# Performance work log

Measured on AMD Instinct MI355X. Metric: run time of the kernel, lower is better.

Reference implementation:

```python
import jax, jax.numpy as jnp
import numpy as np

N_NODES = 100000
N_EDGES = 1600000
NFEAT = 128
NHID = 64
DROPOUT = 0.5


def setup_inputs() -> dict:
    key = jax.random.key(0)
    k1, k2, k3, k4, k5, k6 = jax.random.split(key, 6)
    x = jax.random.normal(k1, (N_NODES, NFEAT), dtype=jnp.float32)
    edge_row = jax.random.randint(k2, (N_EDGES,), 0, N_NODES, dtype=jnp.int32)
    edge_col = jax.random.randint(k3, (N_EDGES,), 0, N_NODES, dtype=jnp.int32)
    edge_val = jax.random.uniform(k4, (N_EDGES,), dtype=jnp.float32)
    # GraphConvolution params (uniform init as in Kipf's reference impl)
    stdv = 1.0 / np.sqrt(NHID)
    W = jax.random.uniform(k5, (NFEAT, NHID), minval=-stdv, maxval=stdv, dtype=jnp.float32)
    b = jax.random.uniform(k6, (NHID,), minval=-stdv, maxval=stdv, dtype=jnp.float32)
    return {"x": x, "edge_row": edge_row, "edge_col": edge_col,
            "edge_val": edge_val, "W": W, "b": b}


def reference(x, edge_row, edge_col, edge_val, W, b):
    # GraphConvolution: support = x @ W ; out = spmm(adj, support) + b
    support = x @ W                                   # [N, nhid]
    msgs = edge_val[:, None] * support[edge_col]       # gather: [E, nhid]
    agg = jax.ops.segment_sum(msgs, edge_row, num_segments=N_NODES)  # scatter-add
    h = jax.nn.relu(agg + b)
    # F.dropout(p=0.5, training=True): inverted dropout with fixed mask
    keep = 1.0 - DROPOUT
    mask = jax.random.bernoulli(jax.random.key(42), keep, h.shape)
    return jnp.where(mask, h / keep, 0.0)
```

## Files before the change

### kernel.cpp

```cpp
#include <hip/hip_runtime.h>

#define N_NODES 100000
#define N_EDGES 1600000
#define NFEAT 128
#define NHID 64

#define BBITS 8
#define NBUCK 391
#define BATCH 4096
#define NBATCH ((N_EDGES + BATCH - 1) / BATCH)
#define CMASK 0x1FFFF

__device__ __forceinline__ unsigned short f2bf(float f) {
  unsigned u = __float_as_uint(f);
  u += 0x7fffu + ((u >> 16) & 1u);
  return (unsigned short)(u >> 16);
}

__global__ __launch_bounds__(256) void gcn_gemm(const float* __restrict__ x,
                                                const float* __restrict__ W,
                                                unsigned short* __restrict__ support_h) {
  __shared__ float lds_x[32 * NFEAT];
  const int t = threadIdx.x;
  const int node0 = blockIdx.x * 32;
  const float4* __restrict__ xg = (const float4*)(x + (size_t)node0 * NFEAT);
  float4* lds4 = (float4*)lds_x;
#pragma unroll
  for (int i = 0; i < 4; ++i)
    lds4[i * 256 + t] = xg[i * 256 + t];
  __syncthreads();
  const int lane = t & 63;
  const int wave = t >> 6;
  const float4* lx = (const float4*)lds_x;
  float acc[8];
#pragma unroll
  for (int n = 0; n < 8; ++n) acc[n] = 0.f;
#pragma unroll 4
  for (int k4 = 0; k4 < NFEAT / 4; ++k4) {
    float wv[4];
#pragma unroll
    for (int j = 0; j < 4; ++j) wv[j] = W[(4 * k4 + j) * NHID + lane];
#pragma unroll
    for (int n = 0; n < 8; ++n) {
      const float4 xv = lx[(wave * 8 + n) * (NFEAT / 4) + k4];
      acc[n] = __builtin_fmaf(xv.x, wv[0], acc[n]);
      acc[n] = __builtin_fmaf(xv.y, wv[1], acc[n]);
      acc[n] = __builtin_fmaf(xv.z, wv[2], acc[n]);
      acc[n] = __builtin_fmaf(xv.w, wv[3], acc[n]);
    }
  }
#pragma unroll
  for (int n = 0; n < 8; ++n)
    support_h[(size_t)(node0 + wave * 8 + n) * NHID + lane] = f2bf(acc[n]);
}

__global__ __launch_bounds__(512) void gcn_bucket_hist(const int* __restrict__ erow,
                                                       int* __restrict__ hist_g) {
  __shared__ int h[NBUCK];
  for (int t = threadIdx.x; t < NBUCK; t += 512) h[t] = 0;
  __syncthreads();
  const int base = blockIdx.x * BATCH;
  const int n = min(BATCH, N_EDGES - base);
  for (int j = threadIdx.x; j < n; j += 512)
    atomicAdd(&h[erow[base + j] >> BBITS], 1);
  __syncthreads();
  for (int t = threadIdx.x; t < NBUCK; t += 512)
    hist_g[(size_t)blockIdx.x * NBUCK + t] = h[t];
}

__global__ __launch_bounds__(512) void gcn_colscan(int* __restrict__ hist_g,
                                                   int* __restrict__ tot) {
  __shared__ int sm[512];
  const int k = blockIdx.x;
  const int t = threadIdx.x;
  const int v = (t < NBATCH) ? hist_g[(size_t)t * NBUCK + k] : 0;
  sm[t] = v;
  __syncthreads();
  for (int off = 1; off < 512; off <<= 1) {
    const int xv = (t >= off) ? sm[t - off] : 0;
    __syncthreads();
    sm[t] += xv;
    __syncthreads();
  }
  if (t < NBATCH) hist_g[(size_t)t * NBUCK + k] = sm[t] - v;
  if (t == NBATCH - 1) tot[k] = sm[t];
}

__global__ __launch_bounds__(512) void gcn_bucket_scan(const int* __restrict__ tot,
                                                       int* __restrict__ bstart,
                                                       int* __restrict__ row_start) {
  __shared__ int sm[512];
  const int t = threadIdx.x;
  const int v = (t < NBUCK) ? tot[t] : 0;
  sm[t] = v;
  __syncthreads();
  for (int off = 1; off < 512; off <<= 1) {
    const int xv = (t >= off) ? sm[t - off] : 0;
    __syncthreads();
    sm[t] += xv;
    __syncthreads();
  }
  if (t < NBUCK) bstart[t] = sm[t] - v;
  if (t == NBUCK - 1) bstart[NBUCK] = sm[t];
  if (t == 0) row_start[N_NODES] = N_EDGES;
}

__global__ __launch_bounds__(512) void gcn_bin(const int* __restrict__ erow,
                                               const int* __restrict__ ecol,
                                               const float* __restrict__ eval_,
                                               const int* __restrict__ colofs,
                                               const int* __restrict__ bstart,
                                               int2* __restrict__ eg) {
  __shared__ int h[NBUCK];
  __shared__ int ofs[NBUCK];
  __shared__ int sm[512];
  __shared__ int spx[BATCH];
  __shared__ int sv[BATCH];
  __shared__ short sb[BATCH];
  const int t = threadIdx.x;
  for (int i = t; i < NBUCK; i += 512) h[i] = 0;
  __syncthreads();
  const int base = blockIdx.x * BATCH;
  const int n = min(BATCH, N_EDGES - base);
  int mypx[8], myv[8], myrank[8], myb[8];
#pragma unroll
  for (int u = 0; u < 8; ++u) {
    const int j = t + u * 512;
    if (j < n) {
      const int r = erow[base + j];
      mypx[u] = ((r & 255) << 17) | ecol[base + j];
      myv[u] = __float_as_int(eval_[base + j]);
      myb[u] = r >> BBITS;
      myrank[u] = atomicAdd(&h[myb[u]], 1);
    }
  }
  __syncthreads();
  const int hv = (t < NBUCK) ? h[t] : 0;
  sm[t] = hv;
  __syncthreads();
  for (int off = 1; off < 512; off <<= 1) {
    const int xv = (t >= off) ? sm[t - off] : 0;
    __syncthreads();
    sm[t] += xv;
    __syncthreads();
  }
  if (t < NBUCK) ofs[t] = sm[t] - hv;
  __syncthreads();
#pragma unroll
  for (int u = 0; u < 8; ++u) {
    const int j = t + u * 512;
    if (j < n) {
      const int pos = ofs[myb[u]] + myrank[u];
      spx[pos] = mypx[u];
      sv[pos] = myv[u];
      sb[pos] = (short)myb[u];
    }
  }
  if (t < NBUCK) h[t] = bstart[t] + colofs[(size_t)blockIdx.x * NBUCK + t] - ofs[t];
  __syncthreads();
  for (int j = t; j < n; j += 512) {
    const int d = h[sb[j]] + j;
    eg[d] = make_int2(spx[j], sv[j]);
  }
}

__global__ __launch_bounds__(512) void gcn_rowsort(const int* __restrict__ bstart,
                                                   int2* __restrict__ eg,
                                                   int* __restrict__ row_start) {
  __shared__ int cnt[256];
  __shared__ int sm[256];
  __shared__ int rofs[256];
  const int t = threadIdx.x;
  const int k = blockIdx.x;
  if (t < 256) cnt[t] = 0;
  __syncthreads();
  const int s = bstart[k];
  const int n = bstart[k + 1] - s;
  int px[9], pv[9], rk[9];
#pragma unroll
  for (int u = 0; u < 9; ++u) {
    const int j = t + u * 512;
    if (j < n) {
      const int2 p = eg[s + j];
      px[u] = p.x;
      pv[u] = p.y;
      rk[u] = atomicAdd(&cnt[p.x >> 17], 1);
    }
  }
  __syncthreads();
  const int myc = (t < 256) ? cnt[t] : 0;
  if (t < 256) sm[t] = myc;
  __syncthreads();
  for (int off = 1; off < 256; off <<= 1) {
    int xv = 0;
    if (t >= off && t < 256) xv = sm[t - off];
    __syncthreads();
    if (t < 256) sm[t] += xv;
    __syncthreads();
  }
  if (t < 256) {
    rofs[t] = sm[t] - myc;
    const int node = (k << BBITS) + t;
    if (node < N_NODES) row_start[node] = s + sm[t] - myc;
  }
  __syncthreads();
#pragma unroll
  for (int u = 0; u < 9; ++u) {
    const int j = t + u * 512;
    if (j < n) {
      const int d = s + rofs[px[u] >> 17] + rk[u];
      eg[d] = make_int2(px[u] & CMASK, pv[u]);
    }
  }
}

__device__ __forceinline__ unsigned rotl32(unsigned v, int r) {
  return (v << r) | (v >> (32 - r));
}

__device__ __forceinline__ unsigned threefry_draw(unsigned i) {
  const unsigned ks0 = 0u;
  const unsigned ks1 = 42u;
  const unsigned ks2 = 0x1BD11BDAu ^ 42u;
  unsigned x0 = 0u + ks0;
  unsigned x1 = i + ks1;
#define TF_ROUND(r) { x0 += x1; x1 = rotl32(x1, (r)); x1 ^= x0; }
  TF_ROUND(13) TF_ROUND(15) TF_ROUND(26) TF_ROUND(6)
  x0 += ks1; x1 += ks2 + 1u;
  TF_ROUND(17) TF_ROUND(29) TF_ROUND(16) TF_ROUND(24)
  x0 += ks2; x1 += ks0 + 2u;
  TF_ROUND(13) TF_ROUND(15) TF_ROUND(26) TF_ROUND(6)
  x0 += ks0; x1 += ks1 + 3u;
  TF_ROUND(17) TF_ROUND(29) TF_ROUND(16) TF_ROUND(24)
  x0 += ks1; x1 += ks2 + 4u;
  TF_ROUND(13) TF_ROUND(15) TF_ROUND(26) TF_ROUND(6)
  x0 += ks2; x1 += ks0 + 5u;
#undef TF_ROUND
  return x0 ^ x1;
}

__global__ __launch_bounds__(256) void gcn_aggregate(const int* __restrict__ row_start,
                                                     const int2* __restrict__ eg,
                                                     const unsigned short* __restrict__ support_h,
                                                     const float* __restrict__ b,
                                                     float* __restrict__ out) {
  const int node = (int)((blockIdx.x * 256u + threadIdx.x) >> 6);
  const int lane = threadIdx.x & 63;
  const int grp = lane >> 3;
  const int sub = lane & 7;
  const int s = row_start[node];
  const int e = row_start[node + 1];
  float acc[8];
#pragma unroll
  for (int j = 0; j < 8; ++j) acc[j] = 0.f;
  for (int i = s; i < e; i += 8) {
    const int idx = i + grp;
    const int2 p = (idx < e) ? eg[idx] : make_int2(0, 0);
    const uint4 q = ((const uint4*)support_h)[(size_t)p.x * 8 + sub];
    const float v = __int_as_float(p.y);
    const float f0 = __uint_as_float(q.x << 16);
    const float f1 = __uint_as_float(q.x & 0xffff0000u);
    const float f2 = __uint_as_float(q.y << 16);
    const float f3 = __uint_as_float(q.y & 0xffff0000u);
    const float f4 = __uint_as_float(q.z << 16);
    const float f5 = __uint_as_float(q.z & 0xffff0000u);
    const float f6 = __uint_as_float(q.w << 16);
    const float f7 = __uint_as_float(q.w & 0xffff0000u);
    acc[0] = __builtin_fmaf(v, f0, acc[0]);
    acc[1] = __builtin_fmaf(v, f1, acc[1]);
    acc[2] = __builtin_fmaf(v, f2, acc[2]);
    acc[3] = __builtin_fmaf(v, f3, acc[3]);
    acc[4] = __builtin_fmaf(v, f4, acc[4]);
    acc[5] = __builtin_fmaf(v, f5, acc[5]);
    acc[6] = __builtin_fmaf(v, f6, acc[6]);
    acc[7] = __builtin_fmaf(v, f7, acc[7]);
  }
#pragma unroll
  for (int m = 8; m <= 32; m <<= 1) {
#pragma unroll
    for (int j = 0; j < 8; ++j) acc[j] += __shfl_xor(acc[j], m);
  }
  const int src = lane >> 3;
  float r[8];
#pragma unroll
  for (int j = 0; j < 8; ++j) r[j] = __shfl(acc[j], src);
  const int js = lane & 7;
  float aval = r[0];
  aval = (js == 1) ? r[1] : aval;
  aval = (js == 2) ? r[2] : aval;
  aval = (js == 3) ? r[3] : aval;
  aval = (js == 4) ? r[4] : aval;
  aval = (js == 5) ? r[5] : aval;
  aval = (js == 6) ? r[6] : aval;
  aval = (js == 7) ? r[7] : aval;
  const float h = fmaxf(aval + b[lane], 0.f);
  const unsigned idxg = (unsigned)node * 64u + (unsigned)lane;
  const bool keep = (threefry_draw(idxg) >> 31) == 0u;
  out[idxg] = keep ? h * 2.0f : 0.0f;
}

extern "C" void kernel_launch(void* const* d_in, const int* in_sizes, int n_in,
                              void* d_out, int out_size, void* d_ws, size_t ws_size,
                              hipStream_t stream) {
  const float* x     = (const float*)d_in[0];
  const int*   erow  = (const int*)d_in[1];
  const int*   ecol  = (const int*)d_in[2];
  const float* eval_ = (const float*)d_in[3];
  const float* W     = (const float*)d_in[4];
  const float* b     = (const float*)d_in[5];
  float* out = (float*)d_out;

  char* ws = (char*)d_ws;
  unsigned short* support_h = (unsigned short*)(ws);
  int2*  eg       = (int2*)(ws + 25600000);
  int*   hist_g   = (int*)(ws + 38400000);
  int*   tot      = (int*)(ws + 39011536);
  int*   bstart   = (int*)(ws + 39013104);
  int*   row_start= (int*)(ws + 39014672);

  hipLaunchKernelGGL(gcn_gemm, dim3(N_NODES / 32), dim3(256), 0, stream, x, W, support_h);
  hipLaunchKernelGGL(gcn_bucket_hist, dim3(NBATCH), dim3(512), 0, stream, erow, hist_g);
  hipLaunchKernelGGL(gcn_colscan, dim3(NBUCK), dim3(512), 0, stream, hist_g, tot);
  hipLaunchKernelGGL(gcn_bucket_scan, dim3(1), dim3(512), 0, stream, tot, bstart, row_start);
  hipLaunchKernelGGL(gcn_bin, dim3(NBATCH), dim3(512), 0, stream,
                     erow, ecol, eval_, hist_g, bstart, eg);
  hipLaunchKernelGGL(gcn_rowsort, dim3(NBUCK), dim3(512), 0, stream,
                     bstart, eg, row_start);
  hipLaunchKernelGGL(gcn_aggregate, dim3(N_NODES / 4), dim3(256), 0, stream,
                     row_start, eg, support_h, b, out);
}
```

Before: 222.5 us.

## Use bf16 MFMA for the dense GEMM and cheaper butterfly reduction in aggregate

Replaces the scalar FMA x@W kernel with a bf16 MFMA 16x16x32 kernel that processes 64 nodes per block, using a pre-transposed bf16 copy of W produced by a new small kernel. Also replaces the aggregate's full shuffle-xor reduction plus broadcast-and-select with a transpose-style butterfly reduction that needs fewer shuffles, with the output feature index permuted to match. Rounding x to bf16 before the multiply adds precision loss, and the extra launch adds a little overhead.

```diff
diff --git a/kernel.cpp b/kernel.cpp
--- a/kernel.cpp
+++ b/kernel.cpp
@@ -11,47 +11,73 @@
 #define NBATCH ((N_EDGES + BATCH - 1) / BATCH)
 #define CMASK 0x1FFFF
 
+typedef __attribute__((ext_vector_type(8))) short short8;
+typedef __attribute__((ext_vector_type(4))) float f32x4;
+
 __device__ __forceinline__ unsigned short f2bf(float f) {
   unsigned u = __float_as_uint(f);
   u += 0x7fffu + ((u >> 16) & 1u);
   return (unsigned short)(u >> 16);
 }
 
+__global__ __launch_bounds__(256) void gcn_wt(const float* __restrict__ W,
+                                              unsigned short* __restrict__ wt) {
+  const int i = blockIdx.x * 256 + threadIdx.x;
+  const int n = i >> 7;
+  const int k = i & 127;
+  wt[i] = f2bf(W[k * NHID + n]);
+}
+
 __global__ __launch_bounds__(256) void gcn_gemm(const float* __restrict__ x,
-                                                const float* __restrict__ W,
+                                                const unsigned short* __restrict__ wt,
                                                 unsigned short* __restrict__ support_h) {
-  __shared__ float lds_x[32 * NFEAT];
-  const int t = threadIdx.x;
-  const int node0 = blockIdx.x * 32;
-  const float4* __restrict__ xg = (const float4*)(x + (size_t)node0 * NFEAT);
-  float4* lds4 = (float4*)lds_x;
-#pragma unroll
-  for (int i = 0; i < 4; ++i)
-    lds4[i * 256 + t] = xg[i * 256 + t];
-  __syncthreads();
+  __shared__ float ldsx[64 * NFEAT];
+  const int t = threadIdx.x;
+  const int node0 = blockIdx.x * 64;
+  const float4* __restrict__ gx = (const float4*)(x + (size_t)node0 * NFEAT);
+  float4* lx4 = (float4*)ldsx;
+  const int limit4 = (N_NODES - node0) * (NFEAT / 4);
+#pragma unroll
+  for (int i = 0; i < 8; ++i) {
+    const int idx = i * 256 + t;
+    if (idx < limit4) lx4[idx] = gx[idx];
+  }
+  __syncthreads();
+  const int wv = t >> 6;
   const int lane = t & 63;
-  const int wave = t >> 6;
-  const float4* lx = (const float4*)lds_x;
-  float acc[8];
-#pragma unroll
-  for (int n = 0; n < 8; ++n) acc[n] = 0.f;
-#pragma unroll 4
-  for (int k4 = 0; k4 < NFEAT / 4; ++k4) {
-    float wv[4];
-#pragma unroll
-    for (int j = 0; j < 4; ++j) wv[j] = W[(4 * k4 + j) * NHID + lane];
-#pragma unroll
-    for (int n = 0; n < 8; ++n) {
-      const float4 xv = lx[(wave * 8 + n) * (NFEAT / 4) + k4];
-      acc[n] = __builtin_fmaf(xv.x, wv[0], acc[n]);
-      acc[n] = __builtin_fmaf(xv.y, wv[1], acc[n]);
-      acc[n] = __builtin_fmaf(xv.z, wv[2], acc[n]);
-      acc[n] = __builtin_fmaf(xv.w, wv[3], acc[n]);
-    }
-  }
-#pragma unroll
-  for (int n = 0; n < 8; ++n)
-    support_h[(size_t)(node0 + wave * 8 + n) * NHID + lane] = f2bf(acc[n]);
+  const int quad = lane >> 4;
+  const int nl = lane & 15;
+  const int mrow = wv * 16 + nl;
+  f32x4 acc[4];
+#pragma unroll
+  for (int nt = 0; nt < 4; ++nt)
+#pragma unroll
+    for (int r = 0; r < 4; ++r) acc[nt][r] = 0.f;
+#pragma unroll
+  for (int kc = 0; kc < 4; ++kc) {
+    const float* ap = &ldsx[mrow * NFEAT + kc * 32 + quad * 8];
+    const float4 a0 = *(const float4*)ap;
+    const float4 a1 = *(const float4*)(ap + 4);
+    union { short8 v; unsigned short s[8]; } au;
+    au.s[0] = f2bf(a0.x); au.s[1] = f2bf(a0.y);
+    au.s[2] = f2bf(a0.z); au.s[3] = f2bf(a0.w);
+    au.s[4] = f2bf(a1.x); au.s[5] = f2bf(a1.y);
+    au.s[6] = f2bf(a1.z); au.s[7] = f2bf(a1.w);
+#pragma unroll
+    for (int nt = 0; nt < 4; ++nt) {
+      const short8 bf = *(const short8*)(wt + (size_t)(nt * 16 + nl) * NFEAT +
+                                         kc * 32 + quad * 8);
+      acc[nt] = __builtin_amdgcn_mfma_f32_16x16x32_bf16(au.v, bf, acc[nt], 0, 0, 0);
+    }
+  }
+#pragma unroll
+  for (int nt = 0; nt < 4; ++nt)
+#pragma unroll
+    for (int r = 0; r < 4; ++r) {
+      const int node = node0 + wv * 16 + quad * 4 + r;
+      if (node < N_NODES)
+        support_h[(size_t)node * NHID + nt * 16 + nl] = f2bf(acc[nt][r]);
+    }
 }
 
 __global__ __launch_bounds__(512) void gcn_bucket_hist(const int* __restrict__ erow,
@@ -258,45 +284,38 @@
     const int2 p = (idx < e) ? eg[idx] : make_int2(0, 0);
     const uint4 q = ((const uint4*)support_h)[(size_t)p.x * 8 + sub];
     const float v = __int_as_float(p.y);
-    const float f0 = __uint_as_float(q.x << 16);
-    const float f1 = __uint_as_float(q.x & 0xffff0000u);
-    const float f2 = __uint_as_float(q.y << 16);
-    const float f3 = __uint_as_float(q.y & 0xffff0000u);
-    const float f4 = __uint_as_float(q.z << 16);
-    const float f5 = __uint_as_float(q.z & 0xffff0000u);
-    const float f6 = __uint_as_float(q.w << 16);
-    const float f7 = __uint_as_float(q.w & 0xffff0000u);
-    acc[0] = __builtin_fmaf(v, f0, acc[0]);
-    acc[1] = __builtin_fmaf(v, f1, acc[1]);
-    acc[2] = __builtin_fmaf(v, f2, acc[2]);
-    acc[3] = __builtin_fmaf(v, f3, acc[3]);
-    acc[4] = __builtin_fmaf(v, f4, acc[4]);
-    acc[5] = __builtin_fmaf(v, f5, acc[5]);
-    acc[6] = __builtin_fmaf(v, f6, acc[6]);
-    acc[7] = __builtin_fmaf(v, f7, acc[7]);
-  }
-#pragma unroll
-  for (int m = 8; m <= 32; m <<= 1) {
-#pragma unroll
-    for (int j = 0; j < 8; ++j) acc[j] += __shfl_xor(acc[j], m);
-  }
-  const int src = lane >> 3;
-  float r[8];
-#pragma unroll
-  for (int j = 0; j < 8; ++j) r[j] = __shfl(acc[j], src);
-  const int js = lane & 7;
-  float aval = r[0];
-  aval = (js == 1) ? r[1] : aval;
-  aval = (js == 2) ? r[2] : aval;
-  aval = (js == 3) ? r[3] : aval;
-  aval = (js == 4) ? r[4] : aval;
-  aval = (js == 5) ? r[5] : aval;
-  aval = (js == 6) ? r[6] : aval;
-  aval = (js == 7) ? r[7] : aval;
-  const float h = fmaxf(aval + b[lane], 0.f);
-  const unsigned idxg = (unsigned)node * 64u + (unsigned)lane;
-  const bool keep = (threefry_draw(idxg) >> 31) == 0u;
-  out[idxg] = keep ? h * 2.0f : 0.0f;
+    acc[0] = __builtin_fmaf(v, __uint_as_float(q.x << 16), acc[0]);
+    acc[1] = __builtin_fmaf(v, __uint_as_float(q.x & 0xffff0000u), acc[1]);
+    acc[2] = __builtin_fmaf(v, __uint_as_float(q.y << 16), acc[2]);
+    acc[3] = __builtin_fmaf(v, __uint_as_float(q.y & 0xffff0000u), acc[3]);
+    acc[4] = __builtin_fmaf(v, __uint_as_float(q.z << 16), acc[4]);
+    acc[5] = __builtin_fmaf(v, __uint_as_float(q.z & 0xffff0000u), acc[5]);
+    acc[6] = __builtin_fmaf(v, __uint_as_float(q.w << 16), acc[6]);
+    acc[7] = __builtin_fmaf(v, __uint_as_float(q.w & 0xffff0000u), acc[7]);
+  }
+  const int g0 = grp & 1, g1 = (grp >> 1) & 1, g2 = grp >> 2;
+  float v4[4];
+#pragma unroll
+  for (int i = 0; i < 4; ++i) {
+    const float keep = g0 ? acc[2 * i + 1] : acc[2 * i];
+    const float give = g0 ? acc[2 * i] : acc[2 * i + 1];
+    v4[i] = keep + __shfl_xor(give, 8);
+  }
+  float v2[2];
+#pragma unroll
+  for (int i = 0; i < 2; ++i) {
+    const float keep = g1 ? v4[2 * i + 1] : v4[2 * i];
+    const float give = g1 ? v4[2 * i] : v4[2 * i + 1];
+    v2[i] = keep + __shfl_xor(give, 16);
+  }
+  const float keep = g2 ? v2[1] : v2[0];
+  const float give = g2 ? v2[0] : v2[1];
+  const float aval = keep + __shfl_xor(give, 32);
+  const int feat = (sub << 3) | grp;
+  const float h = fmaxf(aval + b[feat], 0.f);
+  const unsigned idxg = (unsigned)node * 64u + (unsigned)feat;
+  const bool keepm = (threefry_draw(idxg) >> 31) == 0u;
+  out[idxg] = keepm ? h * 2.0f : 0.0f;
 }
 
 extern "C" void kernel_launch(void* const* d_in, const int* in_sizes, int n_in,
@@ -312,13 +331,16 @@
 
   char* ws = (char*)d_ws;
   unsigned short* support_h = (unsigned short*)(ws);
+  unsigned short* wt        = (unsigned short*)(ws + 12800000);
   int2*  eg       = (int2*)(ws + 25600000);
   int*   hist_g   = (int*)(ws + 38400000);
   int*   tot      = (int*)(ws + 39011536);
   int*   bstart   = (int*)(ws + 39013104);
   int*   row_start= (int*)(ws + 39014672);
 
-  hipLaunchKernelGGL(gcn_gemm, dim3(N_NODES / 32), dim3(256), 0, stream, x, W, support_h);
+  hipLaunchKernelGGL(gcn_wt, dim3(32), dim3(256), 0, stream, W, wt);
+  hipLaunchKernelGGL(gcn_gemm, dim3((N_NODES + 63) / 64), dim3(256), 0, stream,
+                     x, wt, support_h);
   hipLaunchKernelGGL(gcn_bucket_hist, dim3(NBATCH), dim3(512), 0, stream, erow, hist_g);
   hipLaunchKernelGGL(gcn_colscan, dim3(NBUCK), dim3(512), 0, stream, hist_g, tot);
   hipLaunchKernelGGL(gcn_bucket_scan, dim3(1), dim3(512), 0, stream, tot, bstart, row_start);
```

After: 211.6 us. 1.05x faster.
